# Optimization experiments

Measured on AMD Instinct MI355X. Metric: run time of the kernel, lower is better.

## Reference

```python
import jax, jax.numpy as jnp
import numpy as np

B, T, E = 4, 2048, 1024
H, HS = 16, 64  # num_head, head_size; H*HS == E


def setup_inputs() -> dict:
    key = jax.random.key(0)
    ks = jax.random.split(key, 6)
    scale = 0.02
    x = jax.random.normal(ks[0], (B, T, E), dtype=jnp.float32)
    # per-head K/Q/V projection weights, stacked: [H, HS, E] (torch Linear weight layout)
    Wk = jax.random.normal(ks[1], (H, HS, E), dtype=jnp.float32) * scale
    Wq = jax.random.normal(ks[2], (H, HS, E), dtype=jnp.float32) * scale
    Wv = jax.random.normal(ks[3], (H, HS, E), dtype=jnp.float32) * scale
    Wo = jax.random.normal(ks[4], (E, E), dtype=jnp.float32) * scale  # proj weight [out, in]
    bo = jax.random.normal(ks[5], (E,), dtype=jnp.float32) * scale
    return {"x": x, "Wk": Wk, "Wq": Wq, "Wv": Wv, "Wo": Wo, "bo": bo}


def reference(x, Wk, Wq, Wv, Wo, bo):
    # per-head projections: [B,T,H,HS]
    k = jnp.einsum('bte,hde->bthd', x, Wk)
    q = jnp.einsum('bte,hde->bthd', x, Wq)
    v = jnp.einsum('bte,hde->bthd', x, Wv)
    # NOTE: source computes wei = k @ q^T (scores[t,s] = k_t . q_s), reproduced faithfully
    scores = jnp.einsum('bthd,bshd->bhts', k, q) * (HS ** -0.5)  # [B,H,T,T]
    causal = jnp.tril(jnp.ones((T, T), dtype=bool))
    scores = jnp.where(causal[None, None], scores, jnp.float32(-jnp.inf))
    wei = jax.nn.softmax(scores, axis=-1)
    out = jnp.einsum('bhts,bshd->bthd', wei, v)  # [B,T,H,HS]
    out = out.reshape(B, T, H * HS)  # concat heads (head-major order matches torch.cat)
    return out @ Wo.T + bo
```

## Files before the change

### kernel.cpp

```cpp
#include <hip/hip_runtime.h>
#include <hip/hip_bf16.h>
#include <stdint.h>

typedef __attribute__((ext_vector_type(8))) __bf16 bf16x8;
typedef __attribute__((ext_vector_type(4))) float f32x4;
typedef __attribute__((ext_vector_type(16))) float f32x16;
typedef unsigned short u16;

#define MFMA16(a, b, c) __builtin_amdgcn_mfma_f32_16x16x32_bf16((a), (b), (c), 0, 0, 0)
#define MFMA32(a, b, c) __builtin_amdgcn_mfma_f32_32x32x16_bf16((a), (b), (c), 0, 0, 0)

__device__ __forceinline__ u16 f32_to_bf16_rne(float f) {
  union { float f; uint32_t u; } v; v.f = f;
  uint32_t u = v.u;
  u += 0x7fffu + ((u >> 16) & 1u);
  return (u16)(u >> 16);
}

__device__ __forceinline__ void gl_lds16(const void* g, void* l) {
  __builtin_amdgcn_global_load_lds(
      (const __attribute__((address_space(1))) void*)(uintptr_t)g,
      (__attribute__((address_space(3))) void*)(uintptr_t)l,
      16, 0, 0);
}

__device__ __forceinline__ float fast_exp2(float x) {
#if __has_builtin(__builtin_amdgcn_exp2f)
  return __builtin_amdgcn_exp2f(x);
#else
  return exp2f(x);
#endif
}

__device__ __forceinline__ uint32_t cvt_pk_bf16(float a, float b) {
  uint32_t r;
  asm("v_cvt_pk_bf16_f32 %0, %1, %2" : "=v"(r) : "v"(a), "v"(b));
  return r;
}

__global__ void cast_all_kernel(const float* __restrict__ x, const float* __restrict__ Wk,
                                const float* __restrict__ Wq, const float* __restrict__ Wv,
                                const float* __restrict__ Wo, u16* __restrict__ xb,
                                u16* __restrict__ wqkv, u16* __restrict__ wob) {
  const int i = blockIdx.x * 256 + threadIdx.x;
  const float* src; u16* dst; int off;
  if (i < 2097152)      { src = x;  dst = xb;             off = i; }
  else if (i < 2359296) { src = Wk; dst = wqkv;           off = i - 2097152; }
  else if (i < 2621440) { src = Wq; dst = wqkv + 1048576; off = i - 2359296; }
  else if (i < 2883584) { src = Wv; dst = wqkv + 2097152; off = i - 2621440; }
  else                  { src = Wo; dst = wob;            off = i - 2883584; }
  float4 v = reinterpret_cast<const float4*>(src)[off];
  ushort4 o;
  o.x = f32_to_bf16_rne(v.x);
  o.y = f32_to_bf16_rne(v.y);
  o.z = f32_to_bf16_rne(v.z);
  o.w = f32_to_bf16_rne(v.w);
  reinterpret_cast<ushort4*>(dst)[off] = o;
}

template <int FINAL>
__global__ __launch_bounds__(256, 2) void gemm_bt_kernel(
    const u16* __restrict__ A, const u16* __restrict__ Bt,
    void* __restrict__ Cout, const float* __restrict__ bias, int M, int N, int K) {
  __shared__ __attribute__((aligned(16))) u16 As[128 * 32];
  __shared__ __attribute__((aligned(16))) u16 Bs[128 * 32];
  const int tid = threadIdx.x;
  const int lane = tid & 63;
  const int wid = tid >> 6;
  const int wr = wid >> 1, wc = wid & 1;
  const int m0 = blockIdx.y * 128, n0 = blockIdx.x * 128;

  f32x4 acc[4][4] = {};

  const int sr = lane >> 2;
  const int scc = lane & 3;
  const int sh = (sr ^ (sr >> 2)) & 3;
  const int sc = ((scc ^ sh) << 3);
  const int rl = lane & 15;
  const int rh = (rl ^ (rl >> 2)) & 3;
  const int cpr = (((lane >> 4) ^ rh) << 4);

  for (int k0 = 0; k0 < K; k0 += 32) {
    __syncthreads();
#pragma unroll
    for (int i = 0; i < 2; ++i) {
      const int c = wid * 2 + i;
      const int row = c * 16 + sr;
      gl_lds16(A + (size_t)(m0 + row) * K + k0 + sc, (char*)As + c * 1024);
      gl_lds16(Bt + (size_t)(n0 + row) * K + k0 + sc, (char*)Bs + c * 1024);
    }
    __syncthreads();

    bf16x8 af[4], bf[4];
#pragma unroll
    for (int mi = 0; mi < 4; ++mi)
      af[mi] = *(const bf16x8*)((const char*)As + (wr * 64 + mi * 16 + rl) * 64 + cpr);
#pragma unroll
    for (int ni = 0; ni < 4; ++ni)
      bf[ni] = *(const bf16x8*)((const char*)Bs + (wc * 64 + ni * 16 + rl) * 64 + cpr);
    __builtin_amdgcn_s_setprio(1);
#pragma unroll
    for (int mi = 0; mi < 4; ++mi)
#pragma unroll
      for (int ni = 0; ni < 4; ++ni)
        acc[mi][ni] = MFMA16(af[mi], bf[ni], acc[mi][ni]);
    __builtin_amdgcn_s_setprio(0);
  }

#pragma unroll
  for (int mi = 0; mi < 4; ++mi) {
#pragma unroll
    for (int ni = 0; ni < 4; ++ni) {
      const int row = m0 + wr * 64 + mi * 16 + ((lane >> 4) << 2);
      const int col = n0 + wc * 64 + ni * 16 + (lane & 15);
#pragma unroll
      for (int j = 0; j < 4; ++j) {
        if (FINAL) {
          reinterpret_cast<float*>(Cout)[(size_t)(row + j) * N + col] =
              acc[mi][ni][j] + bias[col];
        } else {
          reinterpret_cast<u16*>(Cout)[(size_t)(row + j) * N + col] =
              f32_to_bf16_rne(acc[mi][ni][j]);
        }
      }
    }
  }
}

__device__ __forceinline__ void g256_stage(const u16* __restrict__ src, int b0,
                                           int half, int t, char* region, int K,
                                           int tid) {
  char* dst = region + half * 16384;
  const int w64 = tid & ~63;
  const int lane = tid & 63;
#pragma unroll
  for (int j = 0; j < 2; ++j) {
    const int gbase = j * 512 + w64;
    const int gI = gbase + lane;
    const int r = gI >> 3;
    const int c = ((gI & 7) ^ (r & 7)) * 8;
    gl_lds16(src + (size_t)(b0 + half * 128 + r) * K + t * 64 + c,
             dst + gbase * 16);
  }
}

template <int Q, bool LOADB, int VM>
__device__ __forceinline__ void g256_phase(
    char* lds, int slot, const u16* __restrict__ A, const u16* __restrict__ Bt,
    int m0, int n0, int K, int stT, int stHalf, bool stIsB, int stSlot,
    int wm, int wn, int l15, int l4, int tid,
    bf16x8 (&bf)[2][4], f32x4 (&acc)[8][4]) {
  const char* Ab = lds + slot * 65536 + wm * 16384;
  if (LOADB) {
    const char* Bb = lds + slot * 65536 + 32768 + (wn >> 1) * 16384;
#pragma unroll
    for (int kk = 0; kk < 2; ++kk)
#pragma unroll
      for (int ni = 0; ni < 4; ++ni) {
        const int lr = (wn & 1) * 64 + ni * 16 + l15;
        bf[kk][ni] = *(const bf16x8*)(Bb + lr * 128 + (((kk * 4 + l4) ^ (lr & 7)) << 4));
      }
  }
  bf16x8 af[2][2];
#pragma unroll
  for (int mi = 0; mi < 2; ++mi)
#pragma unroll
    for (int kk = 0; kk < 2; ++kk) {
      const int lr = (Q * 2 + mi) * 16 + l15;
      af[mi][kk] = *(const bf16x8*)(Ab + lr * 128 + (((kk * 4 + l4) ^ (lr & 7)) << 4));
    }
  {
    const u16* src = stIsB ? Bt : A;
    const int b0 = stIsB ? n0 : m0;
    char* region = lds + stSlot * 65536 + (stIsB ? 32768 : 0);
    g256_stage(src, b0, stHalf, stT, region, K, tid);
  }
  if (VM == 4) asm volatile("s_waitcnt vmcnt(4)" ::: "memory");
  __builtin_amdgcn_s_barrier();
  __builtin_amdgcn_s_setprio(1);
#pragma unroll
  for (int mi = 0; mi < 2; ++mi)
#pragma unroll
    for (int ni = 0; ni < 4; ++ni)
#pragma unroll
      for (int kk = 0; kk < 2; ++kk)
        acc[Q * 2 + mi][ni] = MFMA16(af[mi][kk], bf[kk][ni], acc[Q * 2 + mi][ni]);
  __builtin_amdgcn_s_setprio(0);
  __builtin_amdgcn_s_barrier();
}

__global__ __launch_bounds__(512) void gemm256_kernel(
    const u16* __restrict__ A, const u16* __restrict__ Bt, u16* __restrict__ C,
    int M, int N, int K) {
  __shared__ __attribute__((aligned(16))) char lds[131072];

  const int tid = threadIdx.x;
  const int lane = tid & 63;
  const int w = tid >> 6;
  const int wm = w >> 2, wn = w & 3;
  const int l15 = lane & 15, l4 = lane >> 4;

  const int bid = blockIdx.x;
  const int wg = (bid & 7) * (gridDim.x >> 3) + (bid >> 3);
  const int nbx = N >> 8;
  const int by = wg / nbx, bx = wg - by * nbx;
  const int m0 = by << 8, n0 = bx << 8;

  f32x4 acc[8][4] = {};
  bf16x8 bf[2][4];

  g256_stage(A, m0, 0, 0, lds, K, tid);
  g256_stage(A, m0, 1, 0, lds, K, tid);
  g256_stage(Bt, n0, 0, 0, lds + 32768, K, tid);
  g256_stage(Bt, n0, 1, 0, lds + 32768, K, tid);
  g256_stage(Bt, n0, 0, 1, lds + 65536 + 32768, K, tid);
  g256_stage(Bt, n0, 1, 1, lds + 65536 + 32768, K, tid);
  asm volatile("s_waitcnt vmcnt(4)" ::: "memory");
  __builtin_amdgcn_s_barrier();

  const int KT = K >> 6;
#pragma unroll 1
  for (int it = 0; it < (KT >> 1); ++it) {
    const int t1 = it * 2 + 1;
    int t2 = it * 2 + 2; if (t2 > KT - 1) t2 = KT - 1;
    int t3 = it * 2 + 3; if (t3 > KT - 1) t3 = KT - 1;
    g256_phase<0, true, -1>(lds, 0, A, Bt, m0, n0, K, t1, 0, false, 1, wm, wn, l15, l4, tid, bf, acc);
    g256_phase<1, false, -1>(lds, 0, A, Bt, m0, n0, K, t1, 1, false, 1, wm, wn, l15, l4, tid, bf, acc);
    g256_phase<2, false, -1>(lds, 0, A, Bt, m0, n0, K, t2, 0, true, 0, wm, wn, l15, l4, tid, bf, acc);
    g256_phase<3, false, 4>(lds, 0, A, Bt, m0, n0, K, t2, 1, true, 0, wm, wn, l15, l4, tid, bf, acc);
    g256_phase<0, true, -1>(lds, 1, A, Bt, m0, n0, K, t2, 0, false, 0, wm, wn, l15, l4, tid, bf, acc);
    g256_phase<1, false, -1>(lds, 1, A, Bt, m0, n0, K, t2, 1, false, 0, wm, wn, l15, l4, tid, bf, acc);
    g256_phase<2, false, -1>(lds, 1, A, Bt, m0, n0, K, t3, 0, true, 1, wm, wn, l15, l4, tid, bf, acc);
    g256_phase<3, false, 4>(lds, 1, A, Bt, m0, n0, K, t3, 1, true, 1, wm, wn, l15, l4, tid, bf, acc);
  }
  asm volatile("s_waitcnt vmcnt(0)" ::: "memory");

#pragma unroll
  for (int mi = 0; mi < 8; ++mi) {
#pragma unroll
    for (int ni = 0; ni < 4; ++ni) {
      const int row = m0 + wm * 128 + mi * 16 + l4 * 4;
      const int col = n0 + wn * 64 + ni * 16 + l15;
#pragma unroll
      for (int j = 0; j < 4; ++j)
        C[(size_t)(row + j) * N + col] = f32_to_bf16_rne(acc[mi][ni][j]);
    }
  }
}

#define KQVS 3072
#define SCL 0.18033688011f
#define NEG (-1e30f)

__device__ __forceinline__ void v_load(uint4* vr, const u16* __restrict__ Vsrc,
                                       int s0, int tid) {
#pragma unroll
  for (int it = 0; it < 2; ++it) {
    const int idx = it * 256 + tid;
    const int g = idx & 7, srow = idx >> 3;
    vr[it] = *reinterpret_cast<const uint4*>(Vsrc + (size_t)(s0 + srow) * KQVS + g * 8);
  }
}

__device__ __forceinline__ void vt_write(u16* buf, const uint4* vr, int tid) {
#pragma unroll
  for (int it = 0; it < 2; ++it) {
    const int idx = it * 256 + tid;
    const int g = idx & 7, srow = idx >> 3;
    const u16* pv = reinterpret_cast<const u16*>(&vr[it]);
#pragma unroll
    for (int u = 0; u < 8; ++u) {
      const int ue = (u + g) & 7;
      const int d = g * 8 + ue;
      buf[((srow >> 3) * 64 + d) * 8 + (srow & 7)] = pv[ue];
    }
  }
}

__global__ __launch_bounds__(256, 3) void attn_kernel(
    const u16* __restrict__ KQV, u16* __restrict__ Ob) {
  __shared__ __attribute__((aligned(16))) char smem[32768];

  const int tid = threadIdx.x;
  const int lane = tid & 63;
  const int wv = tid >> 6;
  const int l31 = lane & 31;
  const int hh = lane >> 5;
  const bool lolane = (hh == 0);

  const int idx = blockIdx.x;
  const int ttile = 15 - (idx >> 6);
  const int bhpos = idx & 63;
  const int bh = (bhpos & 7) * 8 + (bhpos >> 3);
  const int b = bh >> 4, head = bh & 15;

  const size_t rbase = (size_t)b * 2048;
  const u16* Kh = KQV + rbase * KQVS + head * 64;
  const u16* Qh = Kh + 1024;
  const u16* Vh = Kh + 2048;
  u16* Oh = Ob + rbase * 1024 + head * 64;

  const int t0 = ttile * 128;
  const int nst = 2 * ttile + 2;
  const int t0w = t0 + wv * 32;
  const int tl = t0w + l31;
  const int rb4 = 4 * hh;

#pragma unroll
  for (int i = 0; i < 4; ++i) {
    const int ch = wv * 4 + i;
    const int cc = ch >> 1;
    const int trow = (ch & 1) * 64 + lane;
    gl_lds16(Kh + (size_t)(t0 + trow) * KQVS + cc * 8, smem + 16384 + ch * 1024);
  }
#pragma unroll
  for (int i = 0; i < 2; ++i) {
    const int ch = wv * 2 + i;
    gl_lds16(Qh + (size_t)lane * KQVS + ch * 8, smem + ch * 1024);
  }
  {
    uint4 vr0[2];
    v_load(vr0, Vh, 0, tid);
    vt_write((u16*)(smem + 8192), vr0, tid);
  }
  __syncthreads();

  bf16x8 kf[4];
  {
    const u16* Ksp = (const u16*)(smem + 16384);
#pragma unroll
    for (int kk = 0; kk < 4; ++kk)
      kf[kk] = *(const bf16x8*)(Ksp + ((kk * 2 + hh) * 128 + wv * 32 + l31) * 8);
  }
  __syncthreads();

  f32x16 oa0 = {}, oa1 = {};
  float l_run = 0.f;

#pragma unroll 1
  for (int st = 0; st < nst; ++st) {
    const int cur = st & 1;
    const int s0 = st * 64;
    const bool pref = (st + 1 < nst);
    uint4 vr[2];
    if (pref) {
      v_load(vr, Vh, s0 + 64, tid);
#pragma unroll
      for (int i = 0; i < 2; ++i) {
        const int ch = wv * 2 + i;
        gl_lds16(Qh + (size_t)(s0 + 64 + lane) * KQVS + ch * 8,
                 smem + (cur ^ 1) * 16384 + ch * 1024);
      }
    }

    const bool active = (s0 <= t0w + 31);
    f32x16 sa0 = {}, sa1 = {};
    if (active) {
      if (pref) {
        asm volatile("s_waitcnt vmcnt(4)" ::: "memory");
      } else {
        asm volatile("s_waitcnt vmcnt(0)" ::: "memory");
      }
      __builtin_amdgcn_sched_barrier(0);

      const u16* qb = (const u16*)(smem + cur * 16384);
      __builtin_amdgcn_s_setprio(1);
#pragma unroll
      for (int kk = 0; kk < 4; ++kk) {
        bf16x8 a0 = *(const bf16x8*)(qb + ((kk * 2 + hh) * 64 + l31) * 8);
        bf16x8 a1 = *(const bf16x8*)(qb + ((kk * 2 + hh) * 64 + 32 + l31) * 8);
        sa0 = MFMA32(a0, kf[kk], sa0);
        sa1 = MFMA32(a1, kf[kk], sa1);
      }
      __builtin_amdgcn_s_setprio(0);

      if (s0 + 63 > t0w) {
#pragma unroll
        for (int r = 0; r < 16; ++r) {
          const int rowloc = (r & 3) + 8 * (r >> 2) + rb4;
          if (s0 + rowloc > tl) sa0[r] = NEG;
          if (s0 + 32 + rowloc > tl) sa1[r] = NEG;
        }
      }

#pragma unroll
      for (int r = 0; r < 16; ++r) {
        sa0[r] = fast_exp2(sa0[r] * SCL);
        sa1[r] = fast_exp2(sa1[r] * SCL);
      }
      float rsA = ((sa0[0] + sa0[1]) + (sa0[2] + sa0[3])) +
                  ((sa0[4] + sa0[5]) + (sa0[6] + sa0[7]));
      float rsB = ((sa0[8] + sa0[9]) + (sa0[10] + sa0[11])) +
                  ((sa0[12] + sa0[13]) + (sa0[14] + sa0[15]));
      float rsC = ((sa1[0] + sa1[1]) + (sa1[2] + sa1[3])) +
                  ((sa1[4] + sa1[5]) + (sa1[6] + sa1[7]));
      float rsD = ((sa1[8] + sa1[9]) + (sa1[10] + sa1[11])) +
                  ((sa1[12] + sa1[13]) + (sa1[14] + sa1[15]));
      float rs = (rsA + rsB) + (rsC + rsD);
      rs += __shfl_xor(rs, 32);
      l_run += rs;
    }

    if (pref) vt_write((u16*)(smem + (cur ^ 1) * 16384 + 8192), vr, tid);

    if (active) {
      const u16* vb = (const u16*)(smem + cur * 16384 + 8192);
      __builtin_amdgcn_s_setprio(1);
#define PV_WINDOW(P, r0, w)                                                   \
  {                                                                           \
    uint32_t dA = cvt_pk_bf16(P[r0 + 0], P[r0 + 1]);                          \
    uint32_t dB = cvt_pk_bf16(P[r0 + 2], P[r0 + 3]);                          \
    uint32_t dC = cvt_pk_bf16(P[r0 + 4], P[r0 + 5]);                          \
    uint32_t dD = cvt_pk_bf16(P[r0 + 6], P[r0 + 7]);                          \
    uint32_t sdA = (uint32_t)__shfl_xor((int)dA, 32);                         \
    uint32_t sdB = (uint32_t)__shfl_xor((int)dB, 32);                         \
    uint32_t sdC = (uint32_t)__shfl_xor((int)dC, 32);                         \
    uint32_t sdD = (uint32_t)__shfl_xor((int)dD, 32);                         \
    union { uint32_t u[4]; bf16x8 v; } af;                                    \
    af.u[0] = lolane ? dA : sdC;                                              \
    af.u[1] = lolane ? dB : sdD;                                              \
    af.u[2] = lolane ? sdA : dC;                                              \
    af.u[3] = lolane ? sdB : dD;                                              \
    bf16x8 bv0 = *(const bf16x8*)(vb + ((2 * (w) + hh) * 64 + l31) * 8);      \
    bf16x8 bv1 = *(const bf16x8*)(vb + ((2 * (w) + hh) * 64 + 32 + l31) * 8); \
    oa0 = MFMA32(af.v, bv0, oa0);                                             \
    oa1 = MFMA32(af.v, bv1, oa1);                                             \
  }
      PV_WINDOW(sa0, 0, 0)
      PV_WINDOW(sa0, 8, 1)
      PV_WINDOW(sa1, 0, 2)
      PV_WINDOW(sa1, 8, 3)
#undef PV_WINDOW
      __builtin_amdgcn_s_setprio(0);
    }

    asm volatile("s_waitcnt lgkmcnt(0)" ::: "memory");
    __builtin_amdgcn_s_barrier();
  }

  {
    const float inv = 1.0f / l_run;
#pragma unroll
    for (int r = 0; r < 16; ++r) {
      const int rowloc = (r & 3) + 8 * (r >> 2) + rb4;
      const float ir = __shfl(inv, rowloc);
      const int trow = t0w + rowloc;
      Oh[(size_t)trow * 1024 + l31] = f32_to_bf16_rne(oa0[r] * ir);
      Oh[(size_t)trow * 1024 + 32 + l31] = f32_to_bf16_rne(oa1[r] * ir);
    }
  }
}

extern "C" void kernel_launch(void* const* d_in, const int* in_sizes, int n_in,
                              void* d_out, int out_size, void* d_ws, size_t ws_size,
                              hipStream_t stream) {
  (void)in_sizes; (void)n_in; (void)out_size; (void)ws_size;
  const float* x  = (const float*)d_in[0];
  const float* Wk = (const float*)d_in[1];
  const float* Wq = (const float*)d_in[2];
  const float* Wv = (const float*)d_in[3];
  const float* Wo = (const float*)d_in[4];
  const float* bo = (const float*)d_in[5];
  float* out = (float*)d_out;

  char* ws = (char*)d_ws;
  u16* xb   = (u16*)(ws);
  u16* kqv  = (u16*)(ws + ((size_t)16 << 20));
  u16* wqkv = (u16*)(ws + ((size_t)64 << 20));
  u16* wob  = (u16*)(ws + ((size_t)70 << 20));

  cast_all_kernel<<<dim3(12288), 256, 0, stream>>>(x, Wk, Wq, Wv, Wo, xb, wqkv, wob);

  gemm256_kernel<<<dim3(384), 512, 0, stream>>>(xb, wqkv, kqv, 8192, 3072, 1024);

  attn_kernel<<<dim3(1024), 256, 0, stream>>>(kqv, xb);

  gemm_bt_kernel<1><<<dim3(8, 64), 256, 0, stream>>>(xb, wob, out, bo, 8192, 1024, 1024);
}
```

Measured before the change: 186.2 us.

## Enlarge attention tiles to 256 rows with 512-thread blocks and XCD-aware scheduling

The attention kernel now uses 512-thread blocks (8 waves), each covering 256 query-side rows instead of 128. Each staged 64-row Q/V chunk is therefore shared by twice as many waves, which halves the per-thread load and transpose work. Blocks are remapped so each XCD handles 8 fixed batch-heads, and long and short causal tiles are interleaved to balance load. In exchange there are fewer blocks (512), coarser causal granularity with more idle waves in diagonal tiles, and the occupancy hint of 3 blocks per CU is dropped.

```diff
diff --git a/kernel.cpp b/kernel.cpp
--- a/kernel.cpp
+++ b/kernel.cpp
@@ -252,32 +252,23 @@
 #define SCL 0.18033688011f
 #define NEG (-1e30f)
 
-__device__ __forceinline__ void v_load(uint4* vr, const u16* __restrict__ Vsrc,
-                                       int s0, int tid) {
-#pragma unroll
-  for (int it = 0; it < 2; ++it) {
-    const int idx = it * 256 + tid;
-    const int g = idx & 7, srow = idx >> 3;
-    vr[it] = *reinterpret_cast<const uint4*>(Vsrc + (size_t)(s0 + srow) * KQVS + g * 8);
-  }
-}
-
-__device__ __forceinline__ void vt_write(u16* buf, const uint4* vr, int tid) {
-#pragma unroll
-  for (int it = 0; it < 2; ++it) {
-    const int idx = it * 256 + tid;
-    const int g = idx & 7, srow = idx >> 3;
-    const u16* pv = reinterpret_cast<const u16*>(&vr[it]);
-#pragma unroll
-    for (int u = 0; u < 8; ++u) {
-      const int ue = (u + g) & 7;
-      const int d = g * 8 + ue;
-      buf[((srow >> 3) * 64 + d) * 8 + (srow & 7)] = pv[ue];
-    }
-  }
-}
-
-__global__ __launch_bounds__(256, 3) void attn_kernel(
+__device__ __forceinline__ uint4 v_load1(const u16* __restrict__ Vsrc, int s0, int tid) {
+  const int g = tid & 7, srow = tid >> 3;
+  return *reinterpret_cast<const uint4*>(Vsrc + (size_t)(s0 + srow) * KQVS + g * 8);
+}
+
+__device__ __forceinline__ void vt_write1(u16* buf, uint4 vr, int tid) {
+  const int g = tid & 7, srow = tid >> 3;
+  const u16* pv = reinterpret_cast<const u16*>(&vr);
+#pragma unroll
+  for (int u = 0; u < 8; ++u) {
+    const int ue = (u + g) & 7;
+    const int d = g * 8 + ue;
+    buf[((srow >> 3) * 64 + d) * 8 + (srow & 7)] = pv[ue];
+  }
+}
+
+__global__ __launch_bounds__(512) void attn_kernel(
     const u16* __restrict__ KQV, u16* __restrict__ Ob) {
   __shared__ __attribute__((aligned(16))) char smem[32768];
 
@@ -289,9 +280,12 @@
   const bool lolane = (hh == 0);
 
   const int idx = blockIdx.x;
-  const int ttile = 15 - (idx >> 6);
-  const int bhpos = idx & 63;
-  const int bh = (bhpos & 7) * 8 + (bhpos >> 3);
+  const int xcd = idx & 7;
+  const int pos = idx >> 3;
+  const int qq = (pos < 32) ? pos : (pos - 32);
+  const int bh_loc = qq >> 2;
+  const int p = (pos < 32) ? (7 - (qq & 3)) : (qq & 3);
+  const int bh = xcd * 8 + bh_loc;
   const int b = bh >> 4, head = bh & 15;
 
   const size_t rbase = (size_t)b * 2048;
@@ -300,38 +294,31 @@
   const u16* Vh = Kh + 2048;
   u16* Oh = Ob + rbase * 1024 + head * 64;
 
-  const int t0 = ttile * 128;
-  const int nst = 2 * ttile + 2;
+  const int t0 = p * 256;
+  const int nst = 4 * p + 4;
   const int t0w = t0 + wv * 32;
   const int tl = t0w + l31;
   const int rb4 = 4 * hh;
 
 #pragma unroll
   for (int i = 0; i < 4; ++i) {
-    const int ch = wv * 4 + i;
-    const int cc = ch >> 1;
-    const int trow = (ch & 1) * 64 + lane;
-    gl_lds16(Kh + (size_t)(t0 + trow) * KQVS + cc * 8, smem + 16384 + ch * 1024);
-  }
-#pragma unroll
-  for (int i = 0; i < 2; ++i) {
-    const int ch = wv * 2 + i;
-    gl_lds16(Qh + (size_t)lane * KQVS + ch * 8, smem + ch * 1024);
-  }
-  {
-    uint4 vr0[2];
-    v_load(vr0, Vh, 0, tid);
-    vt_write((u16*)(smem + 8192), vr0, tid);
+    const int c = wv * 4 + i;
+    const int cc = c >> 2;
+    const int trow = (c & 3) * 64 + lane;
+    gl_lds16(Kh + (size_t)(t0 + trow) * KQVS + cc * 8, smem + c * 1024);
   }
   __syncthreads();
-
   bf16x8 kf[4];
   {
-    const u16* Ksp = (const u16*)(smem + 16384);
+    const u16* Ksp = (const u16*)smem;
 #pragma unroll
     for (int kk = 0; kk < 4; ++kk)
-      kf[kk] = *(const bf16x8*)(Ksp + ((kk * 2 + hh) * 128 + wv * 32 + l31) * 8);
-  }
+      kf[kk] = *(const bf16x8*)(Ksp + ((kk * 2 + hh) * 256 + wv * 32 + l31) * 8);
+  }
+  __syncthreads();
+
+  gl_lds16(Qh + (size_t)lane * KQVS + wv * 8, smem + wv * 1024);
+  vt_write1((u16*)(smem + 8192), v_load1(Vh, 0, tid), tid);
   __syncthreads();
 
   f32x16 oa0 = {}, oa1 = {};
@@ -342,22 +329,18 @@
     const int cur = st & 1;
     const int s0 = st * 64;
     const bool pref = (st + 1 < nst);
-    uint4 vr[2];
+    uint4 vr;
     if (pref) {
-      v_load(vr, Vh, s0 + 64, tid);
-#pragma unroll
-      for (int i = 0; i < 2; ++i) {
-        const int ch = wv * 2 + i;
-        gl_lds16(Qh + (size_t)(s0 + 64 + lane) * KQVS + ch * 8,
-                 smem + (cur ^ 1) * 16384 + ch * 1024);
-      }
+      vr = v_load1(Vh, s0 + 64, tid);
+      gl_lds16(Qh + (size_t)(s0 + 64 + lane) * KQVS + wv * 8,
+               smem + (cur ^ 1) * 16384 + wv * 1024);
     }
 
     const bool active = (s0 <= t0w + 31);
     f32x16 sa0 = {}, sa1 = {};
     if (active) {
       if (pref) {
-        asm volatile("s_waitcnt vmcnt(4)" ::: "memory");
+        asm volatile("s_waitcnt vmcnt(2)" ::: "memory");
       } else {
         asm volatile("s_waitcnt vmcnt(0)" ::: "memory");
       }
@@ -401,7 +384,7 @@
       l_run += rs;
     }
 
-    if (pref) vt_write((u16*)(smem + (cur ^ 1) * 16384 + 8192), vr, tid);
+    if (pref) vt_write1((u16*)(smem + (cur ^ 1) * 16384 + 8192), vr, tid);
 
     if (active) {
       const u16* vb = (const u16*)(smem + cur * 16384 + 8192);
@@ -438,6 +421,8 @@
     __builtin_amdgcn_s_barrier();
   }
 
+  asm volatile("s_waitcnt vmcnt(0)" ::: "memory");
+
   {
     const float inv = 1.0f / l_run;
 #pragma unroll
@@ -473,7 +458,7 @@
 
   gemm256_kernel<<<dim3(384), 512, 0, stream>>>(xb, wqkv, kqv, 8192, 3072, 1024);
 
-  attn_kernel<<<dim3(1024), 256, 0, stream>>>(kqv, xb);
+  attn_kernel<<<dim3(512), 512, 0, stream>>>(kqv, xb);
 
   gemm_bt_kernel<1><<<dim3(8, 64), 256, 0, stream>>>(xb, wob, out, bo, 8192, 1024, 1024);
 }
```

Result: slower. 205.9 us (+10.6%).
